# Kernel tuning notes

Hardware: AMD Instinct MI355X
Metric: run time of the kernel (lower is better)

The kernel has to match this reference:

```python
import jax, jax.numpy as jnp
import numpy as np

THRESH = 0.5
TAU = 0.5
GAMMA = 1.0
BETA = 0.9
A = 0.5
B = 0.5


def zif_spike(v):
    # ZIF surrogate: forward is hard threshold (v > 0).
    return (v > 0).astype(v.dtype)


def setup_inputs() -> dict:
    key = jax.random.key(0)
    x = jax.random.normal(key, (64, 8192, 100), dtype=jnp.float32)
    return {"x": x}


def reference(x):
    # x: [B, N, T]; scan over time with (mem, w) state kept per element.
    xt = jnp.moveaxis(x, 2, 0)  # [T, B, N]
    init_mem = jnp.zeros(xt.shape[1:], dtype=x.dtype)
    init_w = jnp.zeros(xt.shape[1:], dtype=x.dtype)

    def step(carry, x_t):
        mem, w = carry
        mem = mem * TAU + x_t - w
        spike = zif_spike(mem - THRESH)
        w = BETA * w + (1.0 - BETA) * (A * mem + B * spike)
        mem = mem - spike * THRESH  # soft reset
        return (mem, w), spike

    _, spikes = jax.lax.scan(step, (init_mem, init_w), xt)  # [T, B, N]
    return jnp.moveaxis(spikes, 0, 2)  # [B, N, T]
```

## Files before the change

### kernel.cpp

```cpp
#include <hip/hip_runtime.h>

#define T_STEPS 100
#define CHUNKS  25
#define TPB     64
#define ELEMS   64
#define TILE_F4 (ELEMS * CHUNKS)
#define GRID    2048

typedef const __attribute__((address_space(1))) unsigned int g_u32;
typedef __attribute__((address_space(3))) unsigned int l_u32;

__global__ __launch_bounds__(TPB) void lif_kernel(const float* __restrict__ x,
                                                  float* __restrict__ out,
                                                  int nt) {
#pragma clang fp contract(off)
    __shared__ float4 tile[2][TILE_F4];

    const int lane = threadIdx.x;
    int t = blockIdx.x;
    if (t >= nt) return;

    {
        const float4* __restrict__ xb = (const float4*)x + (size_t)t * TILE_F4;
#pragma unroll
        for (int k = 0; k < CHUNKS; ++k)
            __builtin_amdgcn_global_load_lds(
                (g_u32*)(xb + k * TPB + lane), (l_u32*)&tile[0][k * TPB], 16, 0, 0);
    }
    asm volatile("s_waitcnt vmcnt(0)" ::: "memory");
    __builtin_amdgcn_sched_barrier(0);

    int buf = 0;
    while (true) {
        const int nxt = t + GRID;
        const bool hn = nxt < nt;

        if (hn) {
            const float4* __restrict__ xb = (const float4*)x + (size_t)nxt * TILE_F4;
#pragma unroll
            for (int k = 0; k < CHUNKS; ++k)
                __builtin_amdgcn_global_load_lds(
                    (g_u32*)(xb + k * TPB + lane),
                    (l_u32*)&tile[buf ^ 1][k * TPB], 16, 0, 0);
        }

        unsigned b0 = 0, b1 = 0, b2 = 0, b3 = 0;
        float mem = 0.0f, wreg = 0.0f;
        const float4* tb = tile[buf];
#pragma unroll
        for (int c = 0; c < CHUNKS; ++c) {
            const float4 xv = tb[lane * CHUNKS + c];
            float xs[4] = {xv.x, xv.y, xv.z, xv.w};
#pragma unroll
            for (int j = 0; j < 4; ++j) {
                mem = (mem * 0.5f + xs[j]) - wreg;
                const bool fire = (mem - 0.5f) > 0.0f;
                const float spike = fire ? 1.0f : 0.0f;
                wreg = 0.9f * wreg + 0.1f * (0.5f * mem + 0.5f * spike);
                mem = mem - spike * 0.5f;
                const int tt = c * 4 + j;
                const unsigned bit = fire ? 1u : 0u;
                if (tt < 32)      b0 |= bit << tt;
                else if (tt < 64) b1 |= bit << (tt - 32);
                else if (tt < 96) b2 |= bit << (tt - 64);
                else              b3 |= bit << (tt - 96);
            }
        }

        float4* __restrict__ ob = (float4*)out + (size_t)t * TILE_F4;
#pragma unroll
        for (int k = 0; k < CHUNKS; ++k) {
            const int f  = k * TPB + lane;
            const int el = f / 25;
            const int c  = f - el * 25;
            const int a  = el << 2;
            const unsigned w0 = (unsigned)__builtin_amdgcn_ds_bpermute(a, (int)b0);
            const unsigned w1 = (unsigned)__builtin_amdgcn_ds_bpermute(a, (int)b1);
            const unsigned w2 = (unsigned)__builtin_amdgcn_ds_bpermute(a, (int)b2);
            const unsigned w3 = (unsigned)__builtin_amdgcn_ds_bpermute(a, (int)b3);
            const unsigned word = (c < 16) ? ((c < 8) ? w0 : w1)
                                           : ((c < 24) ? w2 : w3);
            const int sh = (c & 7) * 4;
            float4 sv;
            sv.x = ((word >> (sh + 0)) & 1u) ? 1.0f : 0.0f;
            sv.y = ((word >> (sh + 1)) & 1u) ? 1.0f : 0.0f;
            sv.z = ((word >> (sh + 2)) & 1u) ? 1.0f : 0.0f;
            sv.w = ((word >> (sh + 3)) & 1u) ? 1.0f : 0.0f;
            ob[f] = sv;
        }

        if (!hn) break;
        asm volatile("s_waitcnt vmcnt(25)" ::: "memory");
        __builtin_amdgcn_sched_barrier(0);
        buf ^= 1;
        t = nxt;
    }
}

extern "C" void kernel_launch(void* const* d_in, const int* in_sizes, int n_in,
                              void* d_out, int out_size, void* d_ws, size_t ws_size,
                              hipStream_t stream) {
    const float* x = (const float*)d_in[0];
    float* out = (float*)d_out;
    int n_elem = in_sizes[0] / T_STEPS;
    int nt = n_elem / ELEMS;
    int grid = nt < GRID ? nt : GRID;

    lif_kernel<<<grid, TPB, 0, stream>>>(x, out, nt);
}
```

Baseline: 365.8 us.

## Launch one block per tile and split input between LDS and registers

Drops the persistent double-buffered loop and launches one 64-thread block per 64-element tile. Each lane loads the last 4 float4 chunks of its own row directly into registers, and the first 21 chunks go through global_load_lds into a single LDS buffer of 21 chunks per row. This shrinks LDS per block so more blocks can be resident to hide latency. The cost is that each block has no prefetch overlap, and the strided direct loads are less coalesced.

New measurement: 346.6 us. 1.06x faster.

```diff
diff --git a/kernel.cpp b/kernel.cpp
--- a/kernel.cpp
+++ b/kernel.cpp
@@ -4,96 +4,90 @@
 #define CHUNKS  25
 #define TPB     64
 #define ELEMS   64
+#define SCH     21
+#define DCH     4
 #define TILE_F4 (ELEMS * CHUNKS)
-#define GRID    2048
+#define SLDS    (ELEMS * SCH)
 
 typedef const __attribute__((address_space(1))) unsigned int g_u32;
 typedef __attribute__((address_space(3))) unsigned int l_u32;
 
 __global__ __launch_bounds__(TPB) void lif_kernel(const float* __restrict__ x,
-                                                  float* __restrict__ out,
-                                                  int nt) {
+                                                  float* __restrict__ out) {
 #pragma clang fp contract(off)
-    __shared__ float4 tile[2][TILE_F4];
+    __shared__ float4 lds[SLDS];
 
     const int lane = threadIdx.x;
-    int t = blockIdx.x;
-    if (t >= nt) return;
+    const float4* __restrict__ xb = (const float4*)x + (size_t)blockIdx.x * TILE_F4;
 
-    {
-        const float4* __restrict__ xb = (const float4*)x + (size_t)t * TILE_F4;
+    float4 dreg[DCH];
 #pragma unroll
-        for (int k = 0; k < CHUNKS; ++k)
-            __builtin_amdgcn_global_load_lds(
-                (g_u32*)(xb + k * TPB + lane), (l_u32*)&tile[0][k * TPB], 16, 0, 0);
+    for (int i = 0; i < DCH; ++i)
+        dreg[i] = xb[lane * CHUNKS + SCH + i];
+
+#pragma unroll
+    for (int k = 0; k < SCH; ++k) {
+        const int s = k * 64 + lane;
+        const int e = s / 21;
+        __builtin_amdgcn_global_load_lds(
+            (g_u32*)(xb + s + 4 * e),
+            (l_u32*)&lds[k * 64], 16, 0, 0);
     }
     asm volatile("s_waitcnt vmcnt(0)" ::: "memory");
     __builtin_amdgcn_sched_barrier(0);
 
-    int buf = 0;
-    while (true) {
-        const int nxt = t + GRID;
-        const bool hn = nxt < nt;
+    unsigned b0 = 0, b1 = 0, b2 = 0, b3 = 0;
+    float mem = 0.0f, wreg = 0.0f;
 
-        if (hn) {
-            const float4* __restrict__ xb = (const float4*)x + (size_t)nxt * TILE_F4;
+#define STEP4(XV, C)                                                        \
+    do {                                                                    \
+        float xs[4] = {(XV).x, (XV).y, (XV).z, (XV).w};                     \
+        _Pragma("unroll")                                                   \
+        for (int j = 0; j < 4; ++j) {                                       \
+            mem = (mem * 0.5f + xs[j]) - wreg;         \
+            const bool fire = (mem - 0.5f) > 0.0f;         \
+            const float spike = fire ? 1.0f : 0.0f;                         \
+            wreg = 0.9f * wreg + 0.1f * (0.5f * mem + 0.5f * spike);        \
+            mem = mem - spike * 0.5f;                       \
+            const int t = (C) * 4 + j;                    \
+            const unsigned bit = fire ? 1u : 0u;                            \
+            if (t < 32)      b0 |= bit << t;                                \
+            else if (t < 64) b1 |= bit << (t - 32);                         \
+            else if (t < 96) b2 |= bit << (t - 64);                         \
+            else             b3 |= bit << (t - 96);                         \
+        }                                                                   \
+    } while (0)
+
 #pragma unroll
-            for (int k = 0; k < CHUNKS; ++k)
-                __builtin_amdgcn_global_load_lds(
-                    (g_u32*)(xb + k * TPB + lane),
-                    (l_u32*)&tile[buf ^ 1][k * TPB], 16, 0, 0);
-        }
+    for (int c = 0; c < SCH; ++c) {
+        const float4 xv = lds[lane * SCH + c];
+        STEP4(xv, c);
+    }
+#pragma unroll
+    for (int i = 0; i < DCH; ++i)
+        STEP4(dreg[i], SCH + i);
+#undef STEP4
 
-        unsigned b0 = 0, b1 = 0, b2 = 0, b3 = 0;
-        float mem = 0.0f, wreg = 0.0f;
-        const float4* tb = tile[buf];
+    float4* __restrict__ ob = (float4*)out + (size_t)blockIdx.x * TILE_F4;
 #pragma unroll
-        for (int c = 0; c < CHUNKS; ++c) {
-            const float4 xv = tb[lane * CHUNKS + c];
-            float xs[4] = {xv.x, xv.y, xv.z, xv.w};
-#pragma unroll
-            for (int j = 0; j < 4; ++j) {
-                mem = (mem * 0.5f + xs[j]) - wreg;
-                const bool fire = (mem - 0.5f) > 0.0f;
-                const float spike = fire ? 1.0f : 0.0f;
-                wreg = 0.9f * wreg + 0.1f * (0.5f * mem + 0.5f * spike);
-                mem = mem - spike * 0.5f;
-                const int tt = c * 4 + j;
-                const unsigned bit = fire ? 1u : 0u;
-                if (tt < 32)      b0 |= bit << tt;
-                else if (tt < 64) b1 |= bit << (tt - 32);
-                else if (tt < 96) b2 |= bit << (tt - 64);
-                else              b3 |= bit << (tt - 96);
-            }
-        }
-
-        float4* __restrict__ ob = (float4*)out + (size_t)t * TILE_F4;
-#pragma unroll
-        for (int k = 0; k < CHUNKS; ++k) {
-            const int f  = k * TPB + lane;
-            const int el = f / 25;
-            const int c  = f - el * 25;
-            const int a  = el << 2;
-            const unsigned w0 = (unsigned)__builtin_amdgcn_ds_bpermute(a, (int)b0);
-            const unsigned w1 = (unsigned)__builtin_amdgcn_ds_bpermute(a, (int)b1);
-            const unsigned w2 = (unsigned)__builtin_amdgcn_ds_bpermute(a, (int)b2);
-            const unsigned w3 = (unsigned)__builtin_amdgcn_ds_bpermute(a, (int)b3);
-            const unsigned word = (c < 16) ? ((c < 8) ? w0 : w1)
-                                           : ((c < 24) ? w2 : w3);
-            const int sh = (c & 7) * 4;
-            float4 sv;
-            sv.x = ((word >> (sh + 0)) & 1u) ? 1.0f : 0.0f;
-            sv.y = ((word >> (sh + 1)) & 1u) ? 1.0f : 0.0f;
-            sv.z = ((word >> (sh + 2)) & 1u) ? 1.0f : 0.0f;
-            sv.w = ((word >> (sh + 3)) & 1u) ? 1.0f : 0.0f;
-            ob[f] = sv;
-        }
-
-        if (!hn) break;
-        asm volatile("s_waitcnt vmcnt(25)" ::: "memory");
-        __builtin_amdgcn_sched_barrier(0);
-        buf ^= 1;
-        t = nxt;
+    for (int k = 0; k < CHUNKS; ++k) {
+        const int f  = k * TPB + lane;
+        const int el = f / 25;
+        const int c  = f - el * 25;
+        const int a  = el << 2;
+        const unsigned w0 = (unsigned)__builtin_amdgcn_ds_bpermute(a, (int)b0);
+        const unsigned w1 = (unsigned)__builtin_amdgcn_ds_bpermute(a, (int)b1);
+        const unsigned w2 = (unsigned)__builtin_amdgcn_ds_bpermute(a, (int)b2);
+        const unsigned w3 = (unsigned)__builtin_amdgcn_ds_bpermute(a, (int)b3);
+        const unsigned word = (c < 16) ? ((c < 8) ? w0 : w1)
+                                       : ((c < 24) ? w2 : w3);
+        const int sh = (c & 7) * 4;
+        float4 sv;
+        sv.x = ((word >> (sh + 0)) & 1u) ? 1.0f : 0.0f;
+        sv.y = ((word >> (sh + 1)) & 1u) ? 1.0f : 0.0f;
+        sv.z = ((word >> (sh + 2)) & 1u) ? 1.0f : 0.0f;
+        sv.w = ((word >> (sh + 3)) & 1u) ? 1.0f : 0.0f;
+        ob[f] = sv;
     }
 }
 
@@ -103,8 +97,7 @@
     const float* x = (const float*)d_in[0];
     float* out = (float*)d_out;
     int n_elem = in_sizes[0] / T_STEPS;
-    int nt = n_elem / ELEMS;
-    int grid = nt < GRID ? nt : GRID;
+    int grid = n_elem / ELEMS;
 
-    lif_kernel<<<grid, TPB, 0, stream>>>(x, out, nt);
+    lif_kernel<<<grid, TPB, 0, stream>>>(x, out);
 }
```
